# Kernel optimization log

Hardware: AMD Instinct MI355X
Metric: run time of the kernel (lower is better)

## Reference

```python
import jax, jax.numpy as jnp
import numpy as np

N = 12288
NUM_DIM = 128
HIDDEN = 16
NUM_CLASS = 16
NEG_BIG = -9e15  # matches torch's -9000000000000000.0 masking constant


def setup_inputs() -> dict:
    key = jax.random.key(0)
    ks = jax.random.split(key, 8)
    scale = 0.1
    return {
        "x": jax.random.normal(ks[0], (N, NUM_DIM), dtype=jnp.float32),
        "W1": jax.random.normal(ks[1], (NUM_DIM, HIDDEN), dtype=jnp.float32) * scale,
        "b1": jnp.zeros((HIDDEN,), dtype=jnp.float32),
        "W2": jax.random.normal(ks[2], (HIDDEN, HIDDEN), dtype=jnp.float32) * scale,
        "b2": jnp.zeros((HIDDEN,), dtype=jnp.float32),
        "W3": jax.random.normal(ks[3], (HIDDEN, NUM_CLASS), dtype=jnp.float32) * scale,
        "b3": jnp.zeros((NUM_CLASS,), dtype=jnp.float32),
    }


def reference(x, W1, b1, W2, b2, W3, b3):
    # Dropout is identity in eval mode; LeakyReLU is defined but never applied.
    h = x @ W1 + b1            # [N, 16]
    h = h @ W2 + b2            # [N, 16]
    h = h @ W3 + b3            # [N, num_class]
    # simAGG: dense similarity, threshold mask, row softmax, re-aggregate.
    adj = h @ h.T                                   # [N, N]
    a = jnp.where(adj > 0, adj, jnp.float32(NEG_BIG))
    sim = jax.nn.softmax(a, axis=1)                 # [N, N]
    out = sim @ h                                   # [N, num_class]
    return jax.nn.log_softmax(out, axis=1)
```

## Files before the change

### kernel.cpp

```cpp
#include <hip/hip_runtime.h>
#include <hip/hip_bf16.h>

#define NROWS 12288
#define NDIM  128
#define HID   16

#define NJC    8
#define JSPAN  (NROWS / NJC)
#define JSTEPS (JSPAN / 32)

typedef float f32x16 __attribute__((ext_vector_type(16)));
typedef short s16x8  __attribute__((ext_vector_type(8)));

__device__ __align__(16) ushort g_hb [NROWS * HID];
__device__ __align__(16) ushort g_hbs[NROWS * HID];
__device__ __align__(16) ushort g_hbT[HID * NROWS];
__device__ float g_pout[(size_t)NJC * NROWS * 16];
__device__ float g_pden[(size_t)NJC * NROWS];

__device__ __forceinline__ ushort f2bf(float f) {
    union { float f; unsigned u; } v; v.f = f;
    unsigned r = v.u + 0x7fffu + ((v.u >> 16) & 1u);
    return (ushort)(r >> 16);
}

#if __has_builtin(__builtin_amdgcn_exp2f)
#define EXP2(x) __builtin_amdgcn_exp2f(x)
#else
#define EXP2(x) exp2f(x)
#endif

__global__ __launch_bounds__(256) void mlp_kernel(
    const float* __restrict__ x,
    const float* __restrict__ W1, const float* __restrict__ b1,
    const float* __restrict__ W2, const float* __restrict__ b2,
    const float* __restrict__ W3, const float* __restrict__ b3)
{
    __shared__ float sW1[NDIM * HID];
    __shared__ float sW2[HID * HID];
    __shared__ float sW3[HID * HID];
    __shared__ float sb[3 * HID];

    const int t = threadIdx.x;
    for (int i = t; i < NDIM * HID; i += 256) sW1[i] = W1[i];
    if (t < HID * HID) { sW2[t] = W2[t]; sW3[t] = W3[t]; }
    if (t < HID) { sb[t] = b1[t]; sb[HID + t] = b2[t]; sb[2 * HID + t] = b3[t]; }
    __syncthreads();

    const int row = blockIdx.x * 256 + t;
    if (row >= NROWS) return;

    float a1[HID];
    #pragma unroll
    for (int c = 0; c < HID; ++c) a1[c] = sb[c];
    const float4* xr = reinterpret_cast<const float4*>(x + (size_t)row * NDIM);
    #pragma unroll 8
    for (int k4 = 0; k4 < NDIM / 4; ++k4) {
        float4 v = xr[k4];
        const float* w0 = &sW1[(k4 * 4 + 0) * HID];
        const float* w1 = &sW1[(k4 * 4 + 1) * HID];
        const float* w2 = &sW1[(k4 * 4 + 2) * HID];
        const float* w3 = &sW1[(k4 * 4 + 3) * HID];
        #pragma unroll
        for (int c = 0; c < HID; ++c)
            a1[c] += v.x * w0[c] + v.y * w1[c] + v.z * w2[c] + v.w * w3[c];
    }

    float a2[HID];
    #pragma unroll
    for (int c = 0; c < HID; ++c) a2[c] = sb[HID + c];
    #pragma unroll
    for (int k = 0; k < HID; ++k) {
        const float hk = a1[k];
        #pragma unroll
        for (int c = 0; c < HID; ++c) a2[c] += hk * sW2[k * HID + c];
    }

    float a3[HID];
    #pragma unroll
    for (int c = 0; c < HID; ++c) a3[c] = sb[2 * HID + c];
    #pragma unroll
    for (int k = 0; k < HID; ++k) {
        const float hk = a2[k];
        #pragma unroll
        for (int c = 0; c < HID; ++c) a3[c] += hk * sW3[k * HID + c];
    }

    ushort hb[HID], hs[HID];
    #pragma unroll
    for (int c = 0; c < HID; ++c) {
        hb[c] = f2bf(a3[c]);
        hs[c] = f2bf(a3[c] * 1.44269504088896f);
    }
    uint wb[8], ws[8];
    #pragma unroll
    for (int d = 0; d < 8; ++d) {
        wb[d] = (uint)hb[2 * d] | ((uint)hb[2 * d + 1] << 16);
        ws[d] = (uint)hs[2 * d] | ((uint)hs[2 * d + 1] << 16);
    }
    uint4* pb = reinterpret_cast<uint4*>(g_hb  + (size_t)row * HID);
    uint4* ps = reinterpret_cast<uint4*>(g_hbs + (size_t)row * HID);
    pb[0] = make_uint4(wb[0], wb[1], wb[2], wb[3]);
    pb[1] = make_uint4(wb[4], wb[5], wb[6], wb[7]);
    ps[0] = make_uint4(ws[0], ws[1], ws[2], ws[3]);
    ps[1] = make_uint4(ws[4], ws[5], ws[6], ws[7]);
    #pragma unroll
    for (int c = 0; c < HID; ++c) g_hbT[(size_t)c * NROWS + row] = hb[c];
}

__global__ __launch_bounds__(256) void agg_kernel()
{
    const int lane = threadIdx.x & 63;
    const int wv   = threadIdx.x >> 6;
    const int jl   = lane & 31;
    const int kh   = lane >> 5;
    const int i0   = blockIdx.x * 128 + wv * 32;
    const int q    = blockIdx.y;
    const int jbase = q * JSPAN;

    const s16x8 bi = *reinterpret_cast<const s16x8*>(&g_hb[((size_t)(i0 + jl)) * HID + kh * 8]);
    const ushort* tcol = &g_hbT[(size_t)(lane & 15) * NROWS];

    f32x16 acc, z;
    #pragma unroll
    for (int r = 0; r < 16; ++r) { acc[r] = 0.0f; z[r] = 0.0f; }
    float dsum = 0.0f;

    for (int js = 0; js < JSTEPS; ++js) {
        const int j0 = jbase + js * 32;

        const s16x8 aj = *reinterpret_cast<const s16x8*>(&g_hbs[((size_t)(j0 + jl)) * HID + kh * 8]);
        f32x16 S = __builtin_amdgcn_mfma_f32_32x32x16_bf16(aj, bi, z, 0, 0, 0);

        float p[16];
        #pragma unroll
        for (int r = 0; r < 16; ++r) {
            const float s  = S[r];
            const float sel = (s > 0.0f) ? s : -200.0f;
            p[r] = EXP2(sel);
            dsum += p[r];
        }

        uint qa, qb, qc, qd;
        asm("v_cvt_pk_bf16_f32 %0, %1, %2" : "=v"(qa) : "v"(p[0]), "v"(p[1]));
        asm("v_cvt_pk_bf16_f32 %0, %1, %2" : "=v"(qb) : "v"(p[2]), "v"(p[3]));
        asm("v_cvt_pk_bf16_f32 %0, %1, %2" : "=v"(qc) : "v"(p[4]), "v"(p[5]));
        asm("v_cvt_pk_bf16_f32 %0, %1, %2" : "=v"(qd) : "v"(p[6]), "v"(p[7]));
        asm volatile("v_permlane32_swap_b32 %0, %1" : "+v"(qa), "+v"(qc));
        asm volatile("v_permlane32_swap_b32 %0, %1" : "+v"(qb), "+v"(qd));
        union { uint u[4]; s16x8 v; } A1;
        A1.u[0] = qa; A1.u[1] = qb; A1.u[2] = qc; A1.u[3] = qd;

        uint qe, qf, qg, qh;
        asm("v_cvt_pk_bf16_f32 %0, %1, %2" : "=v"(qe) : "v"(p[8]),  "v"(p[9]));
        asm("v_cvt_pk_bf16_f32 %0, %1, %2" : "=v"(qf) : "v"(p[10]), "v"(p[11]));
        asm("v_cvt_pk_bf16_f32 %0, %1, %2" : "=v"(qg) : "v"(p[12]), "v"(p[13]));
        asm("v_cvt_pk_bf16_f32 %0, %1, %2" : "=v"(qh) : "v"(p[14]), "v"(p[15]));
        asm volatile("v_permlane32_swap_b32 %0, %1" : "+v"(qe), "+v"(qg));
        asm volatile("v_permlane32_swap_b32 %0, %1" : "+v"(qf), "+v"(qh));
        union { uint u[4]; s16x8 v; } A2;
        A2.u[0] = qe; A2.u[1] = qf; A2.u[2] = qg; A2.u[3] = qh;

        const s16x8 b1 = *reinterpret_cast<const s16x8*>(&tcol[j0 + kh * 8]);
        const s16x8 b2 = *reinterpret_cast<const s16x8*>(&tcol[j0 + 16 + kh * 8]);

        acc = __builtin_amdgcn_mfma_f32_32x32x16_bf16(A1.v, b1, acc, 0, 0, 0);
        acc = __builtin_amdgcn_mfma_f32_32x32x16_bf16(A2.v, b2, acc, 0, 0, 0);
    }

    dsum += __shfl_xor(dsum, 32, 64);
    if (lane < 32) g_pden[(size_t)q * NROWS + i0 + lane] = dsum;

    const int c = lane & 31;
    if (c < 16) {
        #pragma unroll
        for (int r = 0; r < 16; ++r) {
            const int il = (r & 3) + 8 * (r >> 2) + 4 * kh;
            g_pout[((size_t)q * NROWS + (i0 + il)) * 16 + c] = acc[r];
        }
    }
}

__global__ __launch_bounds__(256) void finalize_kernel(float* __restrict__ out)
{
    const int gid = blockIdx.x * 256 + threadIdx.x;
    const int row = gid >> 4;
    const int c   = gid & 15;
    if (row >= NROWS) return;

    float num = 0.0f, den = 0.0f;
    #pragma unroll
    for (int q = 0; q < NJC; ++q) {
        num += g_pout[((size_t)q * NROWS + row) * 16 + c];
        den += g_pden[(size_t)q * NROWS + row];
    }
    const float o = num / den;

    float m = o;
    #pragma unroll
    for (int mask = 1; mask < 16; mask <<= 1) m = fmaxf(m, __shfl_xor(m, mask, 16));
    float e = __expf(o - m), s = e;
    #pragma unroll
    for (int mask = 1; mask < 16; mask <<= 1) s += __shfl_xor(s, mask, 16);

    out[(size_t)row * HID + c] = o - m - __logf(s);
}

extern "C" void kernel_launch(void* const* d_in, const int* in_sizes, int n_in,
                              void* d_out, int out_size, void* d_ws, size_t ws_size,
                              hipStream_t stream) {
    const float* x  = (const float*)d_in[0];
    const float* W1 = (const float*)d_in[1];
    const float* b1 = (const float*)d_in[2];
    const float* W2 = (const float*)d_in[3];
    const float* b2 = (const float*)d_in[4];
    const float* W3 = (const float*)d_in[5];
    const float* b3 = (const float*)d_in[6];
    float* out = (float*)d_out;

    mlp_kernel<<<NROWS / 256, 256, 0, stream>>>(x, W1, b1, W2, b2, W3, b3);
    agg_kernel<<<dim3(NROWS / 128, NJC), 256, 0, stream>>>();
    finalize_kernel<<<(NROWS * 16) / 256, 256, 0, stream>>>(out);
}
```

Measured before the change: 135.1 us.

## Fold softmax denominator into MFMA via ones column, double j-split, shrink MLP blocks

```diff
diff --git a/kernel.cpp b/kernel.cpp
--- a/kernel.cpp
+++ b/kernel.cpp
@@ -5,7 +5,7 @@
 #define NDIM  128
 #define HID   16
 
-#define NJC    8
+#define NJC    16
 #define JSPAN  (NROWS / NJC)
 #define JSTEPS (JSPAN / 32)
 
@@ -14,9 +14,8 @@
 
 __device__ __align__(16) ushort g_hb [NROWS * HID];
 __device__ __align__(16) ushort g_hbs[NROWS * HID];
-__device__ __align__(16) ushort g_hbT[HID * NROWS];
-__device__ float g_pout[(size_t)NJC * NROWS * 16];
-__device__ float g_pden[(size_t)NJC * NROWS];
+__device__ __align__(16) ushort g_hbT[17 * NROWS];
+__device__ float g_pout[(size_t)NJC * NROWS * 17];
 
 __device__ __forceinline__ ushort f2bf(float f) {
     union { float f; unsigned u; } v; v.f = f;
@@ -24,13 +23,15 @@
     return (ushort)(r >> 16);
 }
 
+__device__ __forceinline__ float fast_exp2(float x) {
 #if __has_builtin(__builtin_amdgcn_exp2f)
-#define EXP2(x) __builtin_amdgcn_exp2f(x)
+    return __builtin_amdgcn_exp2f(x);
 #else
-#define EXP2(x) exp2f(x)
+    float r; asm("v_exp_f32 %0, %1" : "=v"(r) : "v"(x)); return r;
 #endif
-
-__global__ __launch_bounds__(256) void mlp_kernel(
+}
+
+__global__ __launch_bounds__(64) void mlp_kernel(
     const float* __restrict__ x,
     const float* __restrict__ W1, const float* __restrict__ b1,
     const float* __restrict__ W2, const float* __restrict__ b2,
@@ -42,12 +43,12 @@
     __shared__ float sb[3 * HID];
 
     const int t = threadIdx.x;
-    for (int i = t; i < NDIM * HID; i += 256) sW1[i] = W1[i];
-    if (t < HID * HID) { sW2[t] = W2[t]; sW3[t] = W3[t]; }
+    for (int i = t; i < NDIM * HID; i += 64) sW1[i] = W1[i];
+    for (int i = t; i < HID * HID; i += 64) { sW2[i] = W2[i]; sW3[i] = W3[i]; }
     if (t < HID) { sb[t] = b1[t]; sb[HID + t] = b2[t]; sb[2 * HID + t] = b3[t]; }
     __syncthreads();
 
-    const int row = blockIdx.x * 256 + t;
+    const int row = blockIdx.x * 64 + t;
     if (row >= NROWS) return;
 
     float a1[HID];
@@ -106,6 +107,7 @@
     ps[1] = make_uint4(ws[4], ws[5], ws[6], ws[7]);
     #pragma unroll
     for (int c = 0; c < HID; ++c) g_hbT[(size_t)c * NROWS + row] = hb[c];
+    g_hbT[(size_t)16 * NROWS + row] = 0x3F80;
 }
 
 __global__ __launch_bounds__(256) void agg_kernel()
@@ -119,12 +121,12 @@
     const int jbase = q * JSPAN;
 
     const s16x8 bi = *reinterpret_cast<const s16x8*>(&g_hb[((size_t)(i0 + jl)) * HID + kh * 8]);
-    const ushort* tcol = &g_hbT[(size_t)(lane & 15) * NROWS];
+    const int ccol = lane & 31;
+    const ushort* tcol = &g_hbT[(size_t)(ccol < 16 ? ccol : 16) * NROWS];
 
     f32x16 acc, z;
     #pragma unroll
     for (int r = 0; r < 16; ++r) { acc[r] = 0.0f; z[r] = 0.0f; }
-    float dsum = 0.0f;
 
     for (int js = 0; js < JSTEPS; ++js) {
         const int j0 = jbase + js * 32;
@@ -135,10 +137,9 @@
         float p[16];
         #pragma unroll
         for (int r = 0; r < 16; ++r) {
-            const float s  = S[r];
+            const float s   = S[r];
             const float sel = (s > 0.0f) ? s : -200.0f;
-            p[r] = EXP2(sel);
-            dsum += p[r];
+            p[r] = fast_exp2(sel);
         }
 
         uint qa, qb, qc, qd;
@@ -146,8 +147,8 @@
         asm("v_cvt_pk_bf16_f32 %0, %1, %2" : "=v"(qb) : "v"(p[2]), "v"(p[3]));
         asm("v_cvt_pk_bf16_f32 %0, %1, %2" : "=v"(qc) : "v"(p[4]), "v"(p[5]));
         asm("v_cvt_pk_bf16_f32 %0, %1, %2" : "=v"(qd) : "v"(p[6]), "v"(p[7]));
-        asm volatile("v_permlane32_swap_b32 %0, %1" : "+v"(qa), "+v"(qc));
-        asm volatile("v_permlane32_swap_b32 %0, %1" : "+v"(qb), "+v"(qd));
+        asm("v_permlane32_swap_b32 %0, %1" : "+v"(qa), "+v"(qc));
+        asm("v_permlane32_swap_b32 %0, %1" : "+v"(qb), "+v"(qd));
         union { uint u[4]; s16x8 v; } A1;
         A1.u[0] = qa; A1.u[1] = qb; A1.u[2] = qc; A1.u[3] = qd;
 
@@ -156,8 +157,8 @@
         asm("v_cvt_pk_bf16_f32 %0, %1, %2" : "=v"(qf) : "v"(p[10]), "v"(p[11]));
         asm("v_cvt_pk_bf16_f32 %0, %1, %2" : "=v"(qg) : "v"(p[12]), "v"(p[13]));
         asm("v_cvt_pk_bf16_f32 %0, %1, %2" : "=v"(qh) : "v"(p[14]), "v"(p[15]));
-        asm volatile("v_permlane32_swap_b32 %0, %1" : "+v"(qe), "+v"(qg));
-        asm volatile("v_permlane32_swap_b32 %0, %1" : "+v"(qf), "+v"(qh));
+        asm("v_permlane32_swap_b32 %0, %1" : "+v"(qe), "+v"(qg));
+        asm("v_permlane32_swap_b32 %0, %1" : "+v"(qf), "+v"(qh));
         union { uint u[4]; s16x8 v; } A2;
         A2.u[0] = qe; A2.u[1] = qf; A2.u[2] = qg; A2.u[3] = qh;
 
@@ -168,15 +169,11 @@
         acc = __builtin_amdgcn_mfma_f32_32x32x16_bf16(A2.v, b2, acc, 0, 0, 0);
     }
 
-    dsum += __shfl_xor(dsum, 32, 64);
-    if (lane < 32) g_pden[(size_t)q * NROWS + i0 + lane] = dsum;
-
-    const int c = lane & 31;
-    if (c < 16) {
+    if (ccol < 17) {
         #pragma unroll
         for (int r = 0; r < 16; ++r) {
             const int il = (r & 3) + 8 * (r >> 2) + 4 * kh;
-            g_pout[((size_t)q * NROWS + (i0 + il)) * 16 + c] = acc[r];
+            g_pout[((size_t)q * NROWS + (i0 + il)) * 17 + ccol] = acc[r];
         }
     }
 }
@@ -191,8 +188,9 @@
     float num = 0.0f, den = 0.0f;
     #pragma unroll
     for (int q = 0; q < NJC; ++q) {
-        num += g_pout[((size_t)q * NROWS + row) * 16 + c];
-        den += g_pden[(size_t)q * NROWS + row];
+        const size_t base = ((size_t)q * NROWS + row) * 17;
+        num += g_pout[base + c];
+        den += g_pout[base + 16];
     }
     const float o = num / den;
 
@@ -218,7 +216,7 @@
     const float* b3 = (const float*)d_in[6];
     float* out = (float*)d_out;
 
-    mlp_kernel<<<NROWS / 256, 256, 0, stream>>>(x, W1, b1, W2, b2, W3, b3);
+    mlp_kernel<<<NROWS / 64, 64, 0, stream>>>(x, W1, b1, W2, b2, W3, b3);
     agg_kernel<<<dim3(NROWS / 128, NJC), 256, 0, stream>>>();
     finalize_kernel<<<(NROWS * 16) / 256, 256, 0, stream>>>(out);
 }
```

Measured after the change: 124.9 us. -7.6%, faster.
